# Optimization experiments

Hardware: AMD Instinct MI355X
Metric: run time of the kernel (lower is better)

Reference implementation:

```python
import jax, jax.numpy as jnp
import numpy as np

E, K, N, T, TOPK, GROUP_SIZE = 8, 2048, 2048, 1024, 2, 128


def setup_inputs() -> dict:
    key = jax.random.key(0)
    ks = jax.random.split(key, 6)
    x = jax.random.normal(ks[0], (T, K), dtype=jnp.float32)
    # uint8-quantized weights stored as int32 (values 0..255)
    w_q = jax.random.randint(ks[1], (E, K, N), 0, 256, dtype=jnp.int32)
    scales = jax.random.uniform(ks[2], (E, K, K // GROUP_SIZE), dtype=jnp.float32) * 0.02
    zeros = jax.random.normal(ks[3], (E, K, K // GROUP_SIZE), dtype=jnp.float32) * 0.1
    topk_weights = jax.random.uniform(ks[4], (T, TOPK), dtype=jnp.float32)
    topk_ids = jax.random.randint(ks[5], (T, TOPK), 0, E, dtype=jnp.int32)
    return {"x": x, "w_q": w_q, "scales": scales, "zeros": zeros,
            "topk_weights": topk_weights, "topk_ids": topk_ids}


def reference(x, w_q, scales, zeros, topk_weights, topk_ids):
    # Faithful to _moe_kernel_w8a16: for each (token, expert-slot) pair,
    #   out[t, n] += topk_weight * sum_k x[t, k] * (w_q[e, k, n] * scales[e, k, k//gs] + zeros[e, k, k//gs])
    # Note the kernel broadcasts scale/zero over n (offs_n * 0) with group index k // group_size.
    k_idx = jnp.arange(K)
    g_idx = k_idx // GROUP_SIZE                      # (K,)
    s = scales[:, k_idx, g_idx]                       # (E, K) scale per (e, k)
    z = zeros[:, k_idx, g_idx]                        # (E, K)
    w_deq = w_q.astype(jnp.float32) * s[:, :, None] + z[:, :, None]  # (E, K, N)
    # dense per-expert GEMM, then gather the top_k experts per token
    all_out = jnp.einsum('tk,ekn->ten', x, w_deq)     # (T, E, N)
    sel = jnp.take_along_axis(all_out, topk_ids[:, :, None].astype(jnp.int32), axis=1)  # (T, TOPK, N)
    out = jnp.sum(sel * topk_weights[:, :, None], axis=1)  # (T, N)
    return out
```

## Files before the change

### kernel.cpp

```cpp
#include <hip/hip_runtime.h>
#include <hip/hip_bf16.h>
#include <stdint.h>

#define E_    8
#define K_    2048
#define N_    2048
#define T_    1024
#define TOPK_ 2
#define NG_   16
#define MAXM  512

#define BM 256
#define BN 64
#define BK 64
#define NST (K_ / BK)
#define MTILES (MAXM / BM)

typedef __attribute__((ext_vector_type(8))) short bf16x8;
typedef __attribute__((ext_vector_type(4))) float f32x4;
typedef __attribute__((ext_vector_type(4))) unsigned int u32x4;
typedef __attribute__((ext_vector_type(8))) unsigned short u16x8;

__device__ __forceinline__ unsigned short f2bf_rne(float f) {
    unsigned u = __float_as_uint(f);
    u += 0x7fffu + ((u >> 16) & 1u);
    return (unsigned short)(u >> 16);
}
__device__ __forceinline__ unsigned short f2bf_trunc(float f) {
    return (unsigned short)(__float_as_uint(f) >> 16);
}

__device__ __forceinline__ void gload_lds16(const void* g, void* l) {
    __builtin_amdgcn_global_load_lds(
        (__attribute__((address_space(1))) unsigned int*)g,
        (__attribute__((address_space(3))) unsigned int*)l,
        16, 0, 0);
}

__global__ void prep_sz(const float* __restrict__ scales, const float* __restrict__ zeros,
                        float* __restrict__ sd, float* __restrict__ zd, int* __restrict__ cnt)
{
    int i = blockIdx.x * 256 + threadIdx.x;
    int e = i >> 11;
    int k = i & (K_ - 1);
    int g = k >> 7;
    size_t src = ((size_t)e * K_ + k) * NG_ + g;
    sd[i] = scales[src];
    zd[i] = zeros[src];
    if (i < E_) cnt[i] = 0;
}

__global__ void route_k(const int* __restrict__ topk_ids, int* __restrict__ cnt,
                        int* __restrict__ ptj)
{
    int idx = blockIdx.x * 256 + threadIdx.x;
    if (idx < T_ * TOPK_) {
        int e = topk_ids[idx];
        int slot = atomicAdd(&cnt[e], 1);
        if (slot < T_ * TOPK_) ptj[e * (T_ * TOPK_) + slot] = idx;
    }
}

__global__ void aprep_k(const float* __restrict__ x, const float* __restrict__ sdiag,
                        const float* __restrict__ zdiag,
                        const int* __restrict__ cnt, const int* __restrict__ ptj,
                        unsigned short* __restrict__ apack, float* __restrict__ zdot)
{
    int e = blockIdx.y;
    int slot = blockIdx.x;
    if (slot >= min(cnt[e], MAXM)) return;
    int tj = ptj[e * (T_ * TOPK_) + slot];
    int t = tj >> 1;
    const float* xr = x + (size_t)t * K_;
    const float* sr = sdiag + (size_t)e * K_;
    const float* zr = zdiag + (size_t)e * K_;
    int k = threadIdx.x * 8;
    f32x4 a0 = *(const f32x4*)(xr + k);
    f32x4 s0 = *(const f32x4*)(sr + k);
    f32x4 a1 = *(const f32x4*)(xr + k + 4);
    f32x4 s1 = *(const f32x4*)(sr + k + 4);
    f32x4 z0 = *(const f32x4*)(zr + k);
    f32x4 z1 = *(const f32x4*)(zr + k + 4);
    u16x8 h;
    h[0] = f2bf_rne(a0.x * s0.x);
    h[1] = f2bf_rne(a0.y * s0.y);
    h[2] = f2bf_rne(a0.z * s0.z);
    h[3] = f2bf_rne(a0.w * s0.w);
    h[4] = f2bf_rne(a1.x * s1.x);
    h[5] = f2bf_rne(a1.y * s1.y);
    h[6] = f2bf_rne(a1.z * s1.z);
    h[7] = f2bf_rne(a1.w * s1.w);
    *(u16x8*)(apack + ((size_t)e * MAXM + slot) * K_ + k) = h;
    float zp = a0.x * z0.x + a0.y * z0.y + a0.z * z0.z + a0.w * z0.w
             + a1.x * z1.x + a1.y * z1.y + a1.z * z1.z + a1.w * z1.w;
#pragma unroll
    for (int off = 32; off > 0; off >>= 1) zp += __shfl_down(zp, off);
    __shared__ float red[4];
    int lane = threadIdx.x & 63;
    int w = threadIdx.x >> 6;
    if (lane == 0) red[w] = zp;
    __syncthreads();
    if (threadIdx.x == 0)
        zdot[tj] = red[0] + red[1] + red[2] + red[3];
}

__global__ __launch_bounds__(512, 2)
void moe_gemm(const int* __restrict__ wq, const unsigned short* __restrict__ apack,
              const float* __restrict__ topk_w, const int* __restrict__ cnt,
              const int* __restrict__ ptj, const float* __restrict__ zdot,
              float* __restrict__ part, float* __restrict__ out, int use_part)
{
    int e = blockIdx.z;
    int count = min(cnt[e], MAXM);
    int m0 = blockIdx.y * BM;
    if (m0 >= count) return;
    int n0 = blockIdx.x * BN;

    __shared__ alignas(16) unsigned short As[2][BM * BK];
    __shared__ alignas(16) unsigned short Bs[2][BN * BK];

    int tid = threadIdx.x;
    int lane = tid & 63;
    int wid = tid >> 6;
    int wm = (wid >> 1) * 64;
    int wn = (wid & 1) * 32;

    int lrow = lane >> 3;
    int lcol = lane & 7;
    int aswz = (lcol ^ lrow) << 4;
    const char* abase = (const char*)(apack + (size_t)e * MAXM * K_);

    int b_n = tid & 63;
    int b_kq = tid >> 6;
    const int* wcol = wq + (size_t)e * K_ * N_ + n0 + b_n;
    int bswz = (b_n & 7) << 4;

    f32x4 acc[4][2] = {};
    int b0[8], b1[8], b2[8];

    auto stageA = [&](int buf, int kt) {
        int kk = kt * BK;
#pragma unroll
        for (int ci = 0; ci < 4; ++ci) {
            int c = wid * 4 + ci;
            int p = m0 + c * 8 + lrow;
            const char* g = abase + ((size_t)p * K_ + kk) * 2 + aswz;
            gload_lds16(g, (char*)As[buf] + c * 1024);
        }
    };
    auto loadB = [&](int* br, int kt) {
        int kb = kt * BK + b_kq * 8;
#pragma unroll
        for (int i = 0; i < 8; ++i)
            br[i] = wcol[(kb + i) * N_];
    };
    auto packB = [&](const int* br, int bbuf) {
        unsigned pk[4];
#pragma unroll
        for (int i = 0; i < 4; ++i) {
            unsigned lo = f2bf_trunc((float)br[2 * i]);
            unsigned hi = f2bf_trunc((float)br[2 * i + 1]);
            pk[i] = lo | (hi << 16);
        }
        char* bsrow = (char*)Bs[bbuf] + b_n * (BK * 2);
        int kbyte = b_kq * 16;
        u32x4 v = { pk[0], pk[1], pk[2], pk[3] };
        *(u32x4*)(bsrow + (kbyte ^ bswz)) = v;
    };
    auto comp = [&](int buf) {
#pragma unroll
        for (int kk2 = 0; kk2 < 2; ++kk2) {
            int kb = kk2 * 64 + ((lane >> 4) << 4);
            bf16x8 af[4], bfr[2];
#pragma unroll
            for (int mi = 0; mi < 4; ++mi) {
                int row = wm + mi * 16 + (lane & 15);
                af[mi] = *(const bf16x8*)((const char*)As[buf] + row * 128 + (kb ^ ((row & 7) << 4)));
            }
#pragma unroll
            for (int ni = 0; ni < 2; ++ni) {
                int row = wn + ni * 16 + (lane & 15);
                bfr[ni] = *(const bf16x8*)((const char*)Bs[buf] + row * 128 + (kb ^ ((row & 7) << 4)));
            }
#pragma unroll
            for (int mi = 0; mi < 4; ++mi)
#pragma unroll
                for (int ni = 0; ni < 2; ++ni)
                    acc[mi][ni] = __builtin_amdgcn_mfma_f32_16x16x32_bf16(
                        af[mi], bfr[ni], acc[mi][ni], 0, 0, 0);
        }
    };

    stageA(0, 0);
    __builtin_amdgcn_sched_barrier(0);
    loadB(b0, 0);
    loadB(b1, 1);
    loadB(b2, 2);
    packB(b0, 0);
    asm volatile("s_waitcnt vmcnt(16) lgkmcnt(0)" ::: "memory");
    __builtin_amdgcn_s_barrier();
    __builtin_amdgcn_sched_barrier(0);

    int kt = 0;
#define STEP(C, BL, BP) do {                                                  \
        stageA(C ^ 1, kt + 1);                                                \
        __builtin_amdgcn_sched_barrier(0);                                    \
        loadB(BL, kt + 3);                                                    \
        comp(C);                                                              \
        packB(BP, C ^ 1);                                                     \
        asm volatile("s_waitcnt vmcnt(8) lgkmcnt(0)" ::: "memory");           \
        __builtin_amdgcn_s_barrier();                                         \
        __builtin_amdgcn_sched_barrier(0);                                    \
        ++kt;                                                                 \
    } while (0)

#pragma unroll 1
    for (int it = 0; it < 4; ++it) {
        STEP(0, b0, b1);
        STEP(1, b1, b2);
        STEP(0, b2, b0);
        STEP(1, b0, b1);
        STEP(0, b1, b2);
        STEP(1, b2, b0);
    }
    STEP(0, b0, b1);
    STEP(1, b1, b2);
    STEP(0, b2, b0);
    STEP(1, b0, b1);
    STEP(0, b1, b2);
#undef STEP
    stageA(0, 30);
    __builtin_amdgcn_sched_barrier(0);
    comp(1);
    packB(b0, 0);
    asm volatile("s_waitcnt vmcnt(0) lgkmcnt(0)" ::: "memory");
    __builtin_amdgcn_s_barrier();
    __builtin_amdgcn_sched_barrier(0);
    stageA(1, 31);
    __builtin_amdgcn_sched_barrier(0);
    comp(0);
    packB(b1, 1);
    asm volatile("s_waitcnt vmcnt(0) lgkmcnt(0)" ::: "memory");
    __builtin_amdgcn_s_barrier();
    __builtin_amdgcn_sched_barrier(0);
    comp(1);

#pragma unroll
    for (int mi = 0; mi < 4; ++mi) {
        int prow = m0 + wm + mi * 16 + ((lane >> 4) << 2);
#pragma unroll
        for (int r = 0; r < 4; ++r) {
            int p = prow + r;
            if (p < count) {
                int tj = ptj[e * (T_ * TOPK_) + p];
                float w = topk_w[tj];
                float zdv = zdot[tj];
                float v0 = w * (acc[mi][0][r] + zdv);
                float v1 = w * (acc[mi][1][r] + zdv);
                if (use_part) {
                    float* pr = part + (size_t)tj * N_ + n0 + wn + (lane & 15);
                    pr[0]  = v0;
                    pr[16] = v1;
                } else {
                    float* orow = out + (size_t)(tj >> 1) * N_ + n0 + wn + (lane & 15);
                    atomicAdd(orow + 0,  v0);
                    atomicAdd(orow + 16, v1);
                }
            }
        }
    }
}

__global__ void reduce_k(const float* __restrict__ part, float* __restrict__ out)
{
    int g = blockIdx.x * 256 + threadIdx.x;
    int t = g >> 9;
    int nc = g & 511;
    f32x4 a = ((const f32x4*)part)[((size_t)(t * 2) << 9) + nc];
    f32x4 b = ((const f32x4*)part)[((size_t)(t * 2 + 1) << 9) + nc];
    ((f32x4*)out)[g] = a + b;
}

extern "C" void kernel_launch(void* const* d_in, const int* in_sizes, int n_in,
                              void* d_out, int out_size, void* d_ws, size_t ws_size,
                              hipStream_t stream)
{
    const float* x       = (const float*)d_in[0];
    const int*   wq      = (const int*)d_in[1];
    const float* scales  = (const float*)d_in[2];
    const float* zeros   = (const float*)d_in[3];
    const float* topk_w  = (const float*)d_in[4];
    const int*   topk_id = (const int*)d_in[5];
    float* out = (float*)d_out;

    char* ws = (char*)d_ws;
    float* sdiag = (float*)(ws + 0);
    float* zdiag = (float*)(ws + 65536);
    int*   cnt   = (int*)(ws + 131072);
    int*   ptj   = (int*)(ws + 135168);
    float* zdot  = (float*)(ws + 200704);
    unsigned short* apack = (unsigned short*)(ws + (1 << 20));
    float* part  = (float*)(ws + ((size_t)17 << 20));
    size_t need = ((size_t)17 << 20) + (size_t)T_ * TOPK_ * N_ * sizeof(float);
    int use_part = (ws_size >= need) ? 1 : 0;

    prep_sz<<<E_ * K_ / 256, 256, 0, stream>>>(scales, zeros, sdiag, zdiag, cnt);
    route_k<<<T_ * TOPK_ / 256, 256, 0, stream>>>(topk_id, cnt, ptj);
    aprep_k<<<dim3(MAXM, E_), 256, 0, stream>>>(x, sdiag, zdiag, cnt, ptj, apack, zdot);
    if (!use_part)
        hipMemsetAsync(d_out, 0, (size_t)T_ * N_ * sizeof(float), stream);
    moe_gemm<<<dim3(N_ / BN, MTILES, E_), 512, 0, stream>>>(
        wq, apack, topk_w, cnt, ptj, zdot, part, out, use_part);
    if (use_part)
        reduce_k<<<T_ * N_ / 4 / 256, 256, 0, stream>>>(part, out);
}
```

Measured before the change: 104.2 us.

## Retile MoE GEMM to 64x128x32 with split-K and row-major B staging

Changes the GEMM tile from 256x64x64 to 64x128x32 with 256-thread blocks, and adds a two-way split-K over the grid z dimension. Partial results go to a doubled partial buffer that the reduce kernel now sums four ways. Weights are loaded as 16-byte int4 vectors along N and stored row-major in LDS with a padded stride; the B fragments are then rebuilt from scalar 16-bit LDS reads. The aim is more blocks for occupancy and coalesced weight reads. In exchange the weights are reloaded for each small M tile, more LDS read instructions are issued, and the partial buffer traffic doubles.

```diff
diff --git a/kernel.cpp b/kernel.cpp
--- a/kernel.cpp
+++ b/kernel.cpp
@@ -10,14 +10,18 @@
 #define NG_   16
 #define MAXM  512
 
-#define BM 256
-#define BN 64
-#define BK 64
-#define NST (K_ / BK)
-#define MTILES (MAXM / BM)
+#define BM 64
+#define BN 128
+#define BK 32
+#define KSPLIT 2
+#define KCHUNK (K_ / KSPLIT)
+#define NST (KCHUNK / BK)
+#define BSTRIDE 132
 
 typedef __attribute__((ext_vector_type(8))) short bf16x8;
 typedef __attribute__((ext_vector_type(4))) float f32x4;
+typedef __attribute__((ext_vector_type(4))) int i32x4;
+typedef __attribute__((ext_vector_type(2))) unsigned int u32x2;
 typedef __attribute__((ext_vector_type(4))) unsigned int u32x4;
 typedef __attribute__((ext_vector_type(8))) unsigned short u16x8;
 
@@ -26,8 +30,9 @@
     u += 0x7fffu + ((u >> 16) & 1u);
     return (unsigned short)(u >> 16);
 }
-__device__ __forceinline__ unsigned short f2bf_trunc(float f) {
-    return (unsigned short)(__float_as_uint(f) >> 16);
+__device__ __forceinline__ unsigned pack2bf(int lo, int hi) {
+    float fl = (float)lo, fh = (float)hi;
+    return (__float_as_uint(fl) >> 16) | (__float_as_uint(fh) & 0xffff0000u);
 }
 
 __device__ __forceinline__ void gload_lds16(const void* g, void* l) {
@@ -104,91 +109,88 @@
         zdot[tj] = red[0] + red[1] + red[2] + red[3];
 }
 
-__global__ __launch_bounds__(512, 2)
+__global__ __launch_bounds__(256, 4)
 void moe_gemm(const int* __restrict__ wq, const unsigned short* __restrict__ apack,
               const float* __restrict__ topk_w, const int* __restrict__ cnt,
               const int* __restrict__ ptj, const float* __restrict__ zdot,
               float* __restrict__ part, float* __restrict__ out, int use_part)
 {
-    int e = blockIdx.z;
+    int bz = blockIdx.z;
+    int e = bz >> 1;
+    int ks = bz & 1;
+    int k0 = ks * KCHUNK;
     int count = min(cnt[e], MAXM);
     int m0 = blockIdx.y * BM;
     if (m0 >= count) return;
     int n0 = blockIdx.x * BN;
 
     __shared__ alignas(16) unsigned short As[2][BM * BK];
-    __shared__ alignas(16) unsigned short Bs[2][BN * BK];
+    __shared__ alignas(16) unsigned short Bs[2][BK * BSTRIDE];
 
     int tid = threadIdx.x;
     int lane = tid & 63;
     int wid = tid >> 6;
-    int wm = (wid >> 1) * 64;
-    int wn = (wid & 1) * 32;
-
-    int lrow = lane >> 3;
-    int lcol = lane & 7;
-    int aswz = (lcol ^ lrow) << 4;
-    const char* abase = (const char*)(apack + (size_t)e * MAXM * K_);
-
-    int b_n = tid & 63;
-    int b_kq = tid >> 6;
-    const int* wcol = wq + (size_t)e * K_ * N_ + n0 + b_n;
-    int bswz = (b_n & 7) << 4;
-
-    f32x4 acc[4][2] = {};
-    int b0[8], b1[8], b2[8];
+    int wm = (wid >> 1) * 32;
+    int wn = (wid & 1) * 64;
+
+    int arow_l = (lane >> 2);
+    int arow = wid * 16 + arow_l;
+    int achk = (lane & 3) ^ (arow & 3);
+    const char* ag = (const char*)(apack + (size_t)e * MAXM * K_)
+                   + ((size_t)(m0 + arow) * K_) * 2 + achk * 16;
+
+    int b_r0 = tid >> 5;
+    int b_c = (tid & 31) * 4;
+    const int* brow = wq + (size_t)e * K_ * N_ + n0 + b_c;
+
+    f32x4 acc[2][4] = {};
+    i32x4 b0[4], b1[4], b2[4];
 
     auto stageA = [&](int buf, int kt) {
-        int kk = kt * BK;
-#pragma unroll
-        for (int ci = 0; ci < 4; ++ci) {
-            int c = wid * 4 + ci;
-            int p = m0 + c * 8 + lrow;
-            const char* g = abase + ((size_t)p * K_ + kk) * 2 + aswz;
-            gload_lds16(g, (char*)As[buf] + c * 1024);
+        const char* g = ag + (size_t)(k0 + kt * BK) * 2;
+        gload_lds16(g, (char*)As[buf] + wid * 1024);
+    };
+    auto loadB = [&](i32x4* br, int kt) {
+        const int* base = brow + (size_t)(k0 + kt * BK + b_r0) * N_;
+#pragma unroll
+        for (int i = 0; i < 4; ++i)
+            br[i] = *(const i32x4*)(base + (size_t)(i * 8) * N_);
+    };
+    auto packB = [&](const i32x4* br, int bbuf) {
+#pragma unroll
+        for (int i = 0; i < 4; ++i) {
+            int row = b_r0 + i * 8;
+            i32x4 v = br[i];
+            u32x2 h = { pack2bf(v.x, v.y), pack2bf(v.z, v.w) };
+            *(u32x2*)(&Bs[bbuf][row * BSTRIDE + b_c]) = h;
         }
     };
-    auto loadB = [&](int* br, int kt) {
-        int kb = kt * BK + b_kq * 8;
-#pragma unroll
-        for (int i = 0; i < 8; ++i)
-            br[i] = wcol[(kb + i) * N_];
-    };
-    auto packB = [&](const int* br, int bbuf) {
-        unsigned pk[4];
-#pragma unroll
-        for (int i = 0; i < 4; ++i) {
-            unsigned lo = f2bf_trunc((float)br[2 * i]);
-            unsigned hi = f2bf_trunc((float)br[2 * i + 1]);
-            pk[i] = lo | (hi << 16);
+    auto comp = [&](int buf) {
+        bf16x8 af[2];
+#pragma unroll
+        for (int mi = 0; mi < 2; ++mi) {
+            int row = wm + mi * 16 + (lane & 15);
+            int kc = (lane >> 4) ^ (row & 3);
+            af[mi] = *(const bf16x8*)((const char*)As[buf] + row * 64 + kc * 16);
         }
-        char* bsrow = (char*)Bs[bbuf] + b_n * (BK * 2);
-        int kbyte = b_kq * 16;
-        u32x4 v = { pk[0], pk[1], pk[2], pk[3] };
-        *(u32x4*)(bsrow + (kbyte ^ bswz)) = v;
-    };
-    auto comp = [&](int buf) {
-#pragma unroll
-        for (int kk2 = 0; kk2 < 2; ++kk2) {
-            int kb = kk2 * 64 + ((lane >> 4) << 4);
-            bf16x8 af[4], bfr[2];
-#pragma unroll
-            for (int mi = 0; mi < 4; ++mi) {
-                int row = wm + mi * 16 + (lane & 15);
-                af[mi] = *(const bf16x8*)((const char*)As[buf] + row * 128 + (kb ^ ((row & 7) << 4)));
-            }
-#pragma unroll
-            for (int ni = 0; ni < 2; ++ni) {
-                int row = wn + ni * 16 + (lane & 15);
-                bfr[ni] = *(const bf16x8*)((const char*)Bs[buf] + row * 128 + (kb ^ ((row & 7) << 4)));
-            }
-#pragma unroll
-            for (int mi = 0; mi < 4; ++mi)
-#pragma unroll
-                for (int ni = 0; ni < 2; ++ni)
-                    acc[mi][ni] = __builtin_amdgcn_mfma_f32_16x16x32_bf16(
-                        af[mi], bfr[ni], acc[mi][ni], 0, 0, 0);
+        bf16x8 bfr[4];
+#pragma unroll
+        for (int ni = 0; ni < 4; ++ni) {
+            int ncol = wn + ni * 16 + (lane & 15);
+            const unsigned short* bp = &Bs[buf][((lane >> 4) * 8) * BSTRIDE + ncol];
+            unsigned d0 = (unsigned)bp[0]           | ((unsigned)bp[BSTRIDE]     << 16);
+            unsigned d1 = (unsigned)bp[2 * BSTRIDE] | ((unsigned)bp[3 * BSTRIDE] << 16);
+            unsigned d2 = (unsigned)bp[4 * BSTRIDE] | ((unsigned)bp[5 * BSTRIDE] << 16);
+            unsigned d3 = (unsigned)bp[6 * BSTRIDE] | ((unsigned)bp[7 * BSTRIDE] << 16);
+            union { unsigned u[4]; bf16x8 v; } f = {{ d0, d1, d2, d3 }};
+            bfr[ni] = f.v;
         }
+#pragma unroll
+        for (int mi = 0; mi < 2; ++mi)
+#pragma unroll
+            for (int ni = 0; ni < 4; ++ni)
+                acc[mi][ni] = __builtin_amdgcn_mfma_f32_16x16x32_bf16(
+                    af[mi], bfr[ni], acc[mi][ni], 0, 0, 0);
     };
 
     stageA(0, 0);
@@ -197,7 +199,7 @@
     loadB(b1, 1);
     loadB(b2, 2);
     packB(b0, 0);
-    asm volatile("s_waitcnt vmcnt(16) lgkmcnt(0)" ::: "memory");
+    asm volatile("s_waitcnt vmcnt(8) lgkmcnt(0)" ::: "memory");
     __builtin_amdgcn_s_barrier();
     __builtin_amdgcn_sched_barrier(0);
 
@@ -208,7 +210,7 @@
         loadB(BL, kt + 3);                                                    \
         comp(C);                                                              \
         packB(BP, C ^ 1);                                                     \
-        asm volatile("s_waitcnt vmcnt(8) lgkmcnt(0)" ::: "memory");           \
+        asm volatile("s_waitcnt vmcnt(4) lgkmcnt(0)" ::: "memory");           \
         __builtin_amdgcn_s_barrier();                                         \
         __builtin_amdgcn_sched_barrier(0);                                    \
         ++kt;                                                                 \
@@ -246,7 +248,7 @@
     comp(1);
 
 #pragma unroll
-    for (int mi = 0; mi < 4; ++mi) {
+    for (int mi = 0; mi < 2; ++mi) {
         int prow = m0 + wm + mi * 16 + ((lane >> 4) << 2);
 #pragma unroll
         for (int r = 0; r < 4; ++r) {
@@ -254,17 +256,15 @@
             if (p < count) {
                 int tj = ptj[e * (T_ * TOPK_) + p];
                 float w = topk_w[tj];
-                float zdv = zdot[tj];
-                float v0 = w * (acc[mi][0][r] + zdv);
-                float v1 = w * (acc[mi][1][r] + zdv);
-                if (use_part) {
-                    float* pr = part + (size_t)tj * N_ + n0 + wn + (lane & 15);
-                    pr[0]  = v0;
-                    pr[16] = v1;
-                } else {
-                    float* orow = out + (size_t)(tj >> 1) * N_ + n0 + wn + (lane & 15);
-                    atomicAdd(orow + 0,  v0);
-                    atomicAdd(orow + 16, v1);
+                float zdv = ks ? 0.f : zdot[tj];
+#pragma unroll
+                for (int ni = 0; ni < 4; ++ni) {
+                    float v = w * (acc[mi][ni][r] + zdv);
+                    int col = n0 + wn + ni * 16 + (lane & 15);
+                    if (use_part)
+                        part[((size_t)tj * 2 + ks) * N_ + col] = v;
+                    else
+                        atomicAdd(out + (size_t)(tj >> 1) * N_ + col, v);
                 }
             }
         }
@@ -276,9 +276,10 @@
     int g = blockIdx.x * 256 + threadIdx.x;
     int t = g >> 9;
     int nc = g & 511;
-    f32x4 a = ((const f32x4*)part)[((size_t)(t * 2) << 9) + nc];
-    f32x4 b = ((const f32x4*)part)[((size_t)(t * 2 + 1) << 9) + nc];
-    ((f32x4*)out)[g] = a + b;
+    const f32x4* p = (const f32x4*)part;
+    size_t base = ((size_t)t * 4) << 9;
+    f32x4 s = p[base + nc] + p[base + 512 + nc] + p[base + 1024 + nc] + p[base + 1536 + nc];
+    ((f32x4*)out)[g] = s;
 }
 
 extern "C" void kernel_launch(void* const* d_in, const int* in_sizes, int n_in,
@@ -301,7 +302,7 @@
     float* zdot  = (float*)(ws + 200704);
     unsigned short* apack = (unsigned short*)(ws + (1 << 20));
     float* part  = (float*)(ws + ((size_t)17 << 20));
-    size_t need = ((size_t)17 << 20) + (size_t)T_ * TOPK_ * N_ * sizeof(float);
+    size_t need = ((size_t)17 << 20) + (size_t)T_ * TOPK_ * KSPLIT * N_ * sizeof(float);
     int use_part = (ws_size >= need) ? 1 : 0;
 
     prep_sz<<<E_ * K_ / 256, 256, 0, stream>>>(scales, zeros, sdiag, zdiag, cnt);
@@ -309,7 +310,7 @@
     aprep_k<<<dim3(MAXM, E_), 256, 0, stream>>>(x, sdiag, zdiag, cnt, ptj, apack, zdot);
     if (!use_part)
         hipMemsetAsync(d_out, 0, (size_t)T_ * N_ * sizeof(float), stream);
-    moe_gemm<<<dim3(N_ / BN, MTILES, E_), 512, 0, stream>>>(
+    moe_gemm<<<dim3(N_ / BN, MAXM / BM, E_ * KSPLIT), 256, 0, stream>>>(
         wq, apack, topk_w, cnt, ptj, zdot, part, out, use_part);
     if (use_part)
         reduce_k<<<T_ * N_ / 4 / 256, 256, 0, stream>>>(part, out);
```

Result: slower. 110.0 us (+5.5%).

## Halve GEMM M-tile to 128 rows and replace partial-sum reduction with atomics

Applied to the files above, without the earlier changes.

The grouped GEMM now uses 128-row M tiles with 256 threads per block. Each thread loads and packs 16 weight rows per K-step instead of 8, and the vmcnt waits are scaled to match. The partial buffer and separate reduce kernel are removed: the output is always zeroed with a memset, and both top-k contributions are accumulated with atomicAdd. This aims for more resident blocks and drops a full write/read of the partial buffer. The cost is more M tiles per expert, so the quantized weights are re-read more often, plus contention on the atomics.

```diff
diff --git a/kernel.cpp b/kernel.cpp
--- a/kernel.cpp
+++ b/kernel.cpp
@@ -10,7 +10,7 @@
 #define NG_   16
 #define MAXM  512
 
-#define BM 256
+#define BM 128
 #define BN 64
 #define BK 64
 #define NST (K_ / BK)
@@ -104,11 +104,11 @@
         zdot[tj] = red[0] + red[1] + red[2] + red[3];
 }
 
-__global__ __launch_bounds__(512, 2)
+__global__ __launch_bounds__(256, 3)
 void moe_gemm(const int* __restrict__ wq, const unsigned short* __restrict__ apack,
               const float* __restrict__ topk_w, const int* __restrict__ cnt,
               const int* __restrict__ ptj, const float* __restrict__ zdot,
-              float* __restrict__ part, float* __restrict__ out, int use_part)
+              float* __restrict__ out)
 {
     int e = blockIdx.z;
     int count = min(cnt[e], MAXM);
@@ -131,12 +131,12 @@
     const char* abase = (const char*)(apack + (size_t)e * MAXM * K_);
 
     int b_n = tid & 63;
-    int b_kq = tid >> 6;
+    int b_set = tid >> 6;
     const int* wcol = wq + (size_t)e * K_ * N_ + n0 + b_n;
     int bswz = (b_n & 7) << 4;
 
     f32x4 acc[4][2] = {};
-    int b0[8], b1[8], b2[8];
+    int b0[16], b1[16], b2[16];
 
     auto stageA = [&](int buf, int kt) {
         int kk = kt * BK;
@@ -149,23 +149,26 @@
         }
     };
     auto loadB = [&](int* br, int kt) {
-        int kb = kt * BK + b_kq * 8;
-#pragma unroll
-        for (int i = 0; i < 8; ++i)
+        int kb = kt * BK + b_set * 16;
+#pragma unroll
+        for (int i = 0; i < 16; ++i)
             br[i] = wcol[(kb + i) * N_];
     };
-    auto packB = [&](const int* br, int bbuf) {
-        unsigned pk[4];
-#pragma unroll
-        for (int i = 0; i < 4; ++i) {
+    auto packB = [&](const int* br, int buf) {
+        unsigned pk[8];
+#pragma unroll
+        for (int i = 0; i < 8; ++i) {
             unsigned lo = f2bf_trunc((float)br[2 * i]);
             unsigned hi = f2bf_trunc((float)br[2 * i + 1]);
             pk[i] = lo | (hi << 16);
         }
-        char* bsrow = (char*)Bs[bbuf] + b_n * (BK * 2);
-        int kbyte = b_kq * 16;
-        u32x4 v = { pk[0], pk[1], pk[2], pk[3] };
-        *(u32x4*)(bsrow + (kbyte ^ bswz)) = v;
+        char* bsrow = (char*)Bs[buf] + b_n * (BK * 2);
+#pragma unroll
+        for (int seg = 0; seg < 2; ++seg) {
+            int kbyte = b_set * 32 + seg * 16;
+            u32x4 v = { pk[seg * 4], pk[seg * 4 + 1], pk[seg * 4 + 2], pk[seg * 4 + 3] };
+            *(u32x4*)(bsrow + (kbyte ^ bswz)) = v;
+        }
     };
     auto comp = [&](int buf) {
 #pragma unroll
@@ -197,7 +200,7 @@
     loadB(b1, 1);
     loadB(b2, 2);
     packB(b0, 0);
-    asm volatile("s_waitcnt vmcnt(16) lgkmcnt(0)" ::: "memory");
+    asm volatile("s_waitcnt vmcnt(32) lgkmcnt(0)" ::: "memory");
     __builtin_amdgcn_s_barrier();
     __builtin_amdgcn_sched_barrier(0);
 
@@ -208,7 +211,7 @@
         loadB(BL, kt + 3);                                                    \
         comp(C);                                                              \
         packB(BP, C ^ 1);                                                     \
-        asm volatile("s_waitcnt vmcnt(8) lgkmcnt(0)" ::: "memory");           \
+        asm volatile("s_waitcnt vmcnt(16) lgkmcnt(0)" ::: "memory");          \
         __builtin_amdgcn_s_barrier();                                         \
         __builtin_amdgcn_sched_barrier(0);                                    \
         ++kt;                                                                 \
@@ -255,30 +258,12 @@
                 int tj = ptj[e * (T_ * TOPK_) + p];
                 float w = topk_w[tj];
                 float zdv = zdot[tj];
-                float v0 = w * (acc[mi][0][r] + zdv);
-                float v1 = w * (acc[mi][1][r] + zdv);
-                if (use_part) {
-                    float* pr = part + (size_t)tj * N_ + n0 + wn + (lane & 15);
-                    pr[0]  = v0;
-                    pr[16] = v1;
-                } else {
-                    float* orow = out + (size_t)(tj >> 1) * N_ + n0 + wn + (lane & 15);
-                    atomicAdd(orow + 0,  v0);
-                    atomicAdd(orow + 16, v1);
-                }
+                float* orow = out + (size_t)(tj >> 1) * N_ + n0 + wn + (lane & 15);
+                atomicAdd(orow + 0,  w * (acc[mi][0][r] + zdv));
+                atomicAdd(orow + 16, w * (acc[mi][1][r] + zdv));
             }
         }
     }
-}
-
-__global__ void reduce_k(const float* __restrict__ part, float* __restrict__ out)
-{
-    int g = blockIdx.x * 256 + threadIdx.x;
-    int t = g >> 9;
-    int nc = g & 511;
-    f32x4 a = ((const f32x4*)part)[((size_t)(t * 2) << 9) + nc];
-    f32x4 b = ((const f32x4*)part)[((size_t)(t * 2 + 1) << 9) + nc];
-    ((f32x4*)out)[g] = a + b;
 }
 
 extern "C" void kernel_launch(void* const* d_in, const int* in_sizes, int n_in,
@@ -300,17 +285,11 @@
     int*   ptj   = (int*)(ws + 135168);
     float* zdot  = (float*)(ws + 200704);
     unsigned short* apack = (unsigned short*)(ws + (1 << 20));
-    float* part  = (float*)(ws + ((size_t)17 << 20));
-    size_t need = ((size_t)17 << 20) + (size_t)T_ * TOPK_ * N_ * sizeof(float);
-    int use_part = (ws_size >= need) ? 1 : 0;
 
     prep_sz<<<E_ * K_ / 256, 256, 0, stream>>>(scales, zeros, sdiag, zdiag, cnt);
     route_k<<<T_ * TOPK_ / 256, 256, 0, stream>>>(topk_id, cnt, ptj);
     aprep_k<<<dim3(MAXM, E_), 256, 0, stream>>>(x, sdiag, zdiag, cnt, ptj, apack, zdot);
-    if (!use_part)
-        hipMemsetAsync(d_out, 0, (size_t)T_ * N_ * sizeof(float), stream);
-    moe_gemm<<<dim3(N_ / BN, MTILES, E_), 512, 0, stream>>>(
-        wq, apack, topk_w, cnt, ptj, zdot, part, out, use_part);
-    if (use_part)
-        reduce_k<<<T_ * N_ / 4 / 256, 256, 0, stream>>>(part, out);
-}
+    hipMemsetAsync(d_out, 0, (size_t)T_ * N_ * sizeof(float), stream);
+    moe_gemm<<<dim3(N_ / BN, MTILES, E_), 256, 0, stream>>>(
+        wq, apack, topk_w, cnt, ptj, zdot, out);
+}
```

New measurement: 85.45 us. 18.0% less time.
